# Optimization experiments

Hardware: AMD Instinct MI355X
Metric: run time of the kernel (lower is better)

The kernel has to match this reference:

```python
import jax, jax.numpy as jnp
import numpy as np

N_NODES = 50000
DEG = 32
HEADS = 4
OUT_F = 16
IN_F = 64
NEG_SLOPE = 0.01  # jax.nn.leaky_relu default


def setup_inputs() -> dict:
    key = jax.random.key(0)
    k_adj, k_mask, k_q, k_qw, k_kw, k_aw = jax.random.split(key, 6)
    adj = jax.random.randint(k_adj, (N_NODES, DEG), 0, N_NODES)
    pad = jax.random.uniform(k_mask, (N_NODES, DEG)) < 0.1
    adj = jnp.where(pad, -1, adj)
    Q = jax.random.normal(k_q, (IN_F, N_NODES), dtype=jnp.float32)
    qw_scale = 2 * np.sqrt(6.0 / (IN_F + OUT_F * HEADS))
    kw_scale = qw_scale
    a_scale = 2 * np.sqrt(6.0 / (OUT_F + HEADS))
    query_weight = (jax.random.uniform(k_qw, (HEADS, OUT_F, IN_F)) - 0.5) * qw_scale
    key_weight = (jax.random.uniform(k_kw, (HEADS, OUT_F, IN_F)) - 0.5) * kw_scale
    attn_weight = (jax.random.uniform(k_aw, (HEADS, OUT_F)) - 0.5) * a_scale
    return {
        'adj': adj,
        'Q': Q,
        'query_weight': query_weight.astype(jnp.float32),
        'key_weight': key_weight.astype(jnp.float32),
        'attn_weight': attn_weight.astype(jnp.float32),
    }


def reference(adj, Q, query_weight, key_weight, attn_weight):
    # K defaults to Q (self-attention over graph)
    K = Q
    # project keys: [H, O, N], then gather neighbors -> [H, O, N, deg]
    Ko = jnp.einsum('hoi,in->hon', key_weight, K)[..., adj]
    # project queries: [H, O, N]
    Qo = jnp.einsum('hoi,in->hon', query_weight, Q)
    # per-edge pre-activation and attention logits
    X = jax.nn.leaky_relu(Qo[..., None] + Ko, negative_slope=NEG_SLOPE)
    X = jnp.einsum('honk,ho->hnk', X, attn_weight)  # [H, N, deg]
    X = jnp.where(adj == -1, -jnp.inf, X)
    # rows with zero valid neighbors -> zero logits (uniform softmax, masked later)
    X = jnp.where((adj != -1).sum(-1, keepdims=True) == 0, 0.0, X)
    attn = jax.nn.softmax(X, axis=-1)
    # weighted aggregate of gathered keys -> [H, O, N]
    return jnp.einsum('hnk,honk->hon', jnp.where(adj == -1, 0.0, attn), Ko)
```

## Files before the change

kernel.cpp:

```cpp
#include <hip/hip_runtime.h>
#include <math.h>

#define DEG 32
#define NHO 64
#define NPW 4
#define NPB 16

typedef short  frag8  __attribute__((ext_vector_type(8)));
typedef float  f32x4  __attribute__((ext_vector_type(4)));

template <int CTRL>
__device__ __forceinline__ float dpp_add(float v) {
    int t = __builtin_amdgcn_update_dpp(0, __float_as_int(v), CTRL, 0xF, 0xF, true);
    return v + __int_as_float(t);
}

__device__ __forceinline__ unsigned bf16_rne(float f) {
    unsigned u = __float_as_uint(f);
    return (u + 0x7fffu + ((u >> 16) & 1u)) >> 16;
}

__global__ __launch_bounds__(256) void proj_mfma_kernel(
    const float* __restrict__ Q,
    const float* __restrict__ Wq,
    const float* __restrict__ Wk,
    unsigned short* __restrict__ Pqb,
    unsigned short* __restrict__ Pkb,
    int N)
{
    __shared__ unsigned qlds[64 * 33];
    __shared__ unsigned wlds[128 * 33];

    int t  = threadIdx.x;
    int n0 = blockIdx.x * 64;

    {
        int l    = t >> 1;
        int half = t & 1;
        const float* wr = (l < 64 ? Wq + (size_t)l * 64
                                  : Wk + (size_t)(l - 64) * 64) + half * 32;
#pragma unroll
        for (int r = 0; r < 16; r++) {
            float f0 = wr[2 * r], f1 = wr[2 * r + 1];
            wlds[l * 33 + half * 16 + r] = bf16_rne(f0) | (bf16_rne(f1) << 16);
        }
    }
    {
        int n  = t & 63;
        int gn = n0 + n;
        bool act = (gn < N);
#pragma unroll
        for (int r = 0; r < 8; r++) {
            int dp = (t >> 6) * 8 + r;
            int k  = dp * 2;
            float f0 = act ? Q[(size_t)k * N + gn] : 0.f;
            float f1 = act ? Q[(size_t)(k + 1) * N + gn] : 0.f;
            qlds[n * 33 + dp] = bf16_rne(f0) | (bf16_rne(f1) << 16);
        }
    }
    __syncthreads();

    int lane = t & 63;
    int w    = t >> 6;
    int li   = lane & 15;
    int quad = lane >> 4;

    f32x4 acc[8];
#pragma unroll
    for (int ot = 0; ot < 8; ot++) acc[ot] = (f32x4){0.f, 0.f, 0.f, 0.f};

#pragma unroll
    for (int ks = 0; ks < 2; ks++) {
        union { unsigned u[4]; frag8 f; } A;
        int abase = (w * 16 + li) * 33 + ks * 16 + quad * 4;
#pragma unroll
        for (int c = 0; c < 4; c++) A.u[c] = qlds[abase + c];
#pragma unroll
        for (int ot = 0; ot < 8; ot++) {
            union { unsigned u[4]; frag8 f; } B;
            int bbase = (ot * 16 + li) * 33 + ks * 16 + quad * 4;
#pragma unroll
            for (int c = 0; c < 4; c++) B.u[c] = wlds[bbase + c];
            acc[ot] = __builtin_amdgcn_mfma_f32_16x16x32_bf16(A.f, B.f, acc[ot],
                                                              0, 0, 0);
        }
    }

#pragma unroll
    for (int ot = 0; ot < 8; ot++) {
#pragma unroll
        for (int r = 0; r < 4; r++) {
            int node = n0 + w * 16 + quad * 4 + r;
            if (node < N) {
                unsigned short v = (unsigned short)bf16_rne(acc[ot][r]);
                if (ot < 4)
                    Pqb[(size_t)node * NHO + ot * 16 + li] = v;
                else
                    Pkb[(size_t)node * NHO + (ot - 4) * 16 + li] = v;
            }
        }
    }
}

__global__ __launch_bounds__(256) void gat_kernel(
    const int*            __restrict__ adj,
    const unsigned short* __restrict__ Pqb,
    const unsigned short* __restrict__ Pkb,
    const float*          __restrict__ aw,
    float*                __restrict__ out,
    int N)
{
    __shared__ float tile[NHO][NPB + 1];

    int l    = threadIdx.x & 63;
    int wv   = threadIdx.x >> 6;
    int sl   = l & 15;
    int slot = l >> 4;

    const uint2* Pk64 = (const uint2*)Pkb;
    const uint2* Pq64 = (const uint2*)Pqb;

    float4 awq = *(const float4*)(aw + 4 * sl);
    const float L2E = 1.44269504f;
    float c1_0 = 0.505f * L2E * awq.x, c2_0 = 0.495f * L2E * awq.x;
    float c1_1 = 0.505f * L2E * awq.y, c2_1 = 0.495f * L2E * awq.y;
    float c1_2 = 0.505f * L2E * awq.z, c2_2 = 0.495f * L2E * awq.z;
    float c1_3 = 0.505f * L2E * awq.w, c2_3 = 0.495f * L2E * awq.w;

    int bprm_x16 = (l ^ 16) * 4;
    int bprm_x32 = (l ^ 32) * 4;

    int nbase = blockIdx.x * NPB + wv * NPW;

#pragma unroll 1
    for (int ni = 0; ni < NPW; ni++) {
        int n = nbase + ni;
        if (n < N) {
            uint2 qraw = Pq64[(size_t)n * 16 + sl];
            float qp0 = __uint_as_float(qraw.x << 16);
            float qp1 = __uint_as_float(qraw.x & 0xffff0000u);
            float qp2 = __uint_as_float(qraw.y << 16);
            float qp3 = __uint_as_float(qraw.y & 0xffff0000u);
            int adjA  = adj[(size_t)n * DEG + (l & 31)];

            float c1q = c1_0 * qp0;
            c1q = fmaf(c1_1, qp1, c1q);
            c1q = fmaf(c1_2, qp2, c1q);
            c1q = fmaf(c1_3, qp3, c1q);

            int   jv[8];
            uint2 kvr[8];
#pragma unroll
            for (int t = 0; t < 8; t++) {
                int j = __builtin_amdgcn_ds_bpermute((slot * 8 + t) * 4, adjA);
                jv[t] = j;
                kvr[t] = Pk64[(size_t)(j < 0 ? 0 : j) * 16 + sl];
            }

            float s = 0.f, a0 = 0.f, a1 = 0.f, a2 = 0.f, a3 = 0.f;
#pragma unroll
            for (int t = 0; t < 8; t++) {
                float kv0 = __uint_as_float(kvr[t].x << 16);
                float kv1 = __uint_as_float(kvr[t].x & 0xffff0000u);
                float kv2 = __uint_as_float(kvr[t].y << 16);
                float kv3 = __uint_as_float(kvr[t].y & 0xffff0000u);
                float x0 = qp0 + kv0, x1 = qp1 + kv1;
                float x2 = qp2 + kv2, x3 = qp3 + kv3;
                float c = fmaf(c1_0, kv0, c1q);
                c = fmaf(c1_1, kv1, c);
                c = fmaf(c1_2, kv2, c);
                c = fmaf(c1_3, kv3, c);
                c = fmaf(c2_0, fabsf(x0), c);
                c = fmaf(c2_1, fabsf(x1), c);
                c = fmaf(c2_2, fabsf(x2), c);
                c = fmaf(c2_3, fabsf(x3), c);
                c = dpp_add<0xB1>(c);
                c = dpp_add<0x4E>(c);
                float p = __builtin_amdgcn_exp2f(c);
                p = (jv[t] >= 0) ? p : 0.f;
                s += p;
                a0 = fmaf(p, kv0, a0);
                a1 = fmaf(p, kv1, a1);
                a2 = fmaf(p, kv2, a2);
                a3 = fmaf(p, kv3, a3);
            }

            s  += __int_as_float(__builtin_amdgcn_ds_bpermute(bprm_x16, __float_as_int(s)));
            a0 += __int_as_float(__builtin_amdgcn_ds_bpermute(bprm_x16, __float_as_int(a0)));
            a1 += __int_as_float(__builtin_amdgcn_ds_bpermute(bprm_x16, __float_as_int(a1)));
            a2 += __int_as_float(__builtin_amdgcn_ds_bpermute(bprm_x16, __float_as_int(a2)));
            a3 += __int_as_float(__builtin_amdgcn_ds_bpermute(bprm_x16, __float_as_int(a3)));
            s  += __int_as_float(__builtin_amdgcn_ds_bpermute(bprm_x32, __float_as_int(s)));
            a0 += __int_as_float(__builtin_amdgcn_ds_bpermute(bprm_x32, __float_as_int(a0)));
            a1 += __int_as_float(__builtin_amdgcn_ds_bpermute(bprm_x32, __float_as_int(a1)));
            a2 += __int_as_float(__builtin_amdgcn_ds_bpermute(bprm_x32, __float_as_int(a2)));
            a3 += __int_as_float(__builtin_amdgcn_ds_bpermute(bprm_x32, __float_as_int(a3)));

            float rs = (s > 0.f) ? __builtin_amdgcn_rcpf(s) : 0.f;
            if (slot == 0) {
                int col = wv * NPW + ni;
                tile[4 * sl + 0][col] = a0 * rs;
                tile[4 * sl + 1][col] = a1 * rs;
                tile[4 * sl + 2][col] = a2 * rs;
                tile[4 * sl + 3][col] = a3 * rs;
            }
        }
    }
    __syncthreads();

    int n0 = blockIdx.x * NPB;
    int lr = threadIdx.x >> 2;
    int c4 = threadIdx.x & 3;
    int nc = n0 + c4 * 4;
    float4 v = make_float4(tile[lr][c4 * 4 + 0], tile[lr][c4 * 4 + 1],
                           tile[lr][c4 * 4 + 2], tile[lr][c4 * 4 + 3]);
    if (nc + 3 < N) {
        *(float4*)(out + (size_t)lr * N + nc) = v;
    } else {
#pragma unroll
        for (int e = 0; e < 4; e++)
            if (nc + e < N) out[(size_t)lr * N + nc + e] = (&v.x)[e];
    }
}

extern "C" void kernel_launch(void* const* d_in, const int* in_sizes, int n_in,
                              void* d_out, int out_size, void* d_ws, size_t ws_size,
                              hipStream_t stream) {
    const int*   adj = (const int*)  d_in[0];
    const float* Q   = (const float*)d_in[1];
    const float* qw  = (const float*)d_in[2];
    const float* kw  = (const float*)d_in[3];
    const float* aw  = (const float*)d_in[4];
    float*       out = (float*)d_out;

    int N = in_sizes[0] / DEG;

    unsigned short* Pqb = (unsigned short*)d_ws;
    unsigned short* Pkb = Pqb + (size_t)N * NHO;

    proj_mfma_kernel<<<(N + 63) / 64, 256, 0, stream>>>(Q, qw, kw, Pqb, Pkb, N);

    gat_kernel<<<(N + NPB - 1) / NPB, 256, 0, stream>>>(adj, Pqb, Pkb, aw, out, N);
}
```

Measured before the change: 109.5 us.

## Double-buffer neighbor gathers and load adjacency as int4 in GAT kernel

The per-wave node loop is unrolled and the neighbor key gathers are double-buffered, so the next node's Pk loads are in flight while the current node computes. Adjacency indices are now loaded directly as two int4 vectors per lane instead of one scalar load followed by eight ds_bpermute shuffles. The xor-16 reduction step uses ds_swizzle instead of bpermute, and launch bounds request 4 blocks per CU. The cost is higher register pressure from the two 8-entry gather buffers and the preloaded indices, which could limit occupancy.

```diff
diff --git a/kernel.cpp b/kernel.cpp
--- a/kernel.cpp
+++ b/kernel.cpp
@@ -102,7 +102,96 @@
     }
 }
 
-__global__ __launch_bounds__(256) void gat_kernel(
+
+__device__ __forceinline__ float swz_x16(float v) {
+    return __int_as_float(__builtin_amdgcn_ds_swizzle(__float_as_int(v), 0x401F));
+}
+__device__ __forceinline__ float bprm(int addr, float v) {
+    return __int_as_float(__builtin_amdgcn_ds_bpermute(addr, __float_as_int(v)));
+}
+
+__device__ __forceinline__ void gat_gather(uint2 (&dst)[8],
+                                           const int4 lo, const int4 hi,
+                                           const uint2* __restrict__ Pk64,
+                                           int sl) {
+    dst[0] = Pk64[(size_t)(lo.x < 0 ? 0 : lo.x) * 16 + sl];
+    dst[1] = Pk64[(size_t)(lo.y < 0 ? 0 : lo.y) * 16 + sl];
+    dst[2] = Pk64[(size_t)(lo.z < 0 ? 0 : lo.z) * 16 + sl];
+    dst[3] = Pk64[(size_t)(lo.w < 0 ? 0 : lo.w) * 16 + sl];
+    dst[4] = Pk64[(size_t)(hi.x < 0 ? 0 : hi.x) * 16 + sl];
+    dst[5] = Pk64[(size_t)(hi.y < 0 ? 0 : hi.y) * 16 + sl];
+    dst[6] = Pk64[(size_t)(hi.z < 0 ? 0 : hi.z) * 16 + sl];
+    dst[7] = Pk64[(size_t)(hi.w < 0 ? 0 : hi.w) * 16 + sl];
+}
+
+__device__ __forceinline__ void gat_compute(
+    const uint2 (&kv)[8], const int4 lo, const int4 hi, uint2 qraw,
+    float c1_0, float c1_1, float c1_2, float c1_3,
+    float c2_0, float c2_1, float c2_2, float c2_3,
+    int slot, int sl, int bprm_x32, int col,
+    float (&tile)[NHO][NPB + 1])
+{
+    float qp0 = __uint_as_float(qraw.x << 16);
+    float qp1 = __uint_as_float(qraw.x & 0xffff0000u);
+    float qp2 = __uint_as_float(qraw.y << 16);
+    float qp3 = __uint_as_float(qraw.y & 0xffff0000u);
+
+    float c1q = c1_0 * qp0;
+    c1q = fmaf(c1_1, qp1, c1q);
+    c1q = fmaf(c1_2, qp2, c1q);
+    c1q = fmaf(c1_3, qp3, c1q);
+
+    const int jt[8] = {lo.x, lo.y, lo.z, lo.w, hi.x, hi.y, hi.z, hi.w};
+
+    float s = 0.f, a0 = 0.f, a1 = 0.f, a2 = 0.f, a3 = 0.f;
+#pragma unroll
+    for (int t = 0; t < 8; t++) {
+        float kv0 = __uint_as_float(kv[t].x << 16);
+        float kv1 = __uint_as_float(kv[t].x & 0xffff0000u);
+        float kv2 = __uint_as_float(kv[t].y << 16);
+        float kv3 = __uint_as_float(kv[t].y & 0xffff0000u);
+        float x0 = qp0 + kv0, x1 = qp1 + kv1;
+        float x2 = qp2 + kv2, x3 = qp3 + kv3;
+        float c = fmaf(c1_0, kv0, c1q);
+        c = fmaf(c1_1, kv1, c);
+        c = fmaf(c1_2, kv2, c);
+        c = fmaf(c1_3, kv3, c);
+        c = fmaf(c2_0, fabsf(x0), c);
+        c = fmaf(c2_1, fabsf(x1), c);
+        c = fmaf(c2_2, fabsf(x2), c);
+        c = fmaf(c2_3, fabsf(x3), c);
+        c = dpp_add<0xB1>(c);
+        c = dpp_add<0x4E>(c);
+        float p = __builtin_amdgcn_exp2f(c);
+        p = (jt[t] >= 0) ? p : 0.f;
+        s += p;
+        a0 = fmaf(p, kv0, a0);
+        a1 = fmaf(p, kv1, a1);
+        a2 = fmaf(p, kv2, a2);
+        a3 = fmaf(p, kv3, a3);
+    }
+
+    s  += swz_x16(s);
+    a0 += swz_x16(a0);
+    a1 += swz_x16(a1);
+    a2 += swz_x16(a2);
+    a3 += swz_x16(a3);
+    s  += bprm(bprm_x32, s);
+    a0 += bprm(bprm_x32, a0);
+    a1 += bprm(bprm_x32, a1);
+    a2 += bprm(bprm_x32, a2);
+    a3 += bprm(bprm_x32, a3);
+
+    float rs = (s > 0.f) ? __builtin_amdgcn_rcpf(s) : 0.f;
+    if (slot == 0) {
+        tile[4 * sl + 0][col] = a0 * rs;
+        tile[4 * sl + 1][col] = a1 * rs;
+        tile[4 * sl + 2][col] = a2 * rs;
+        tile[4 * sl + 3][col] = a3 * rs;
+    }
+}
+
+__global__ __launch_bounds__(256, 4) void gat_kernel(
     const int*            __restrict__ adj,
     const unsigned short* __restrict__ Pqb,
     const unsigned short* __restrict__ Pkb,
@@ -127,82 +216,54 @@
     float c1_2 = 0.505f * L2E * awq.z, c2_2 = 0.495f * L2E * awq.z;
     float c1_3 = 0.505f * L2E * awq.w, c2_3 = 0.495f * L2E * awq.w;
 
-    int bprm_x16 = (l ^ 16) * 4;
     int bprm_x32 = (l ^ 32) * 4;
-
     int nbase = blockIdx.x * NPB + wv * NPW;
 
+    if (nbase + NPW <= N) {
+        int4  aLo[NPW], aHi[NPW];
+        uint2 qr[NPW];
+#pragma unroll
+        for (int ni = 0; ni < NPW; ni++) {
+            const int* ap = adj + (size_t)(nbase + ni) * DEG + slot * 8;
+            aLo[ni] = *(const int4*)ap;
+            aHi[ni] = *(const int4*)(ap + 4);
+            qr[ni]  = Pq64[(size_t)(nbase + ni) * 16 + sl];
+        }
+
+        uint2 kvA[8], kvB[8];
+        gat_gather(kvA, aLo[0], aHi[0], Pk64, sl);
+
+#pragma unroll
+        for (int ni = 0; ni < NPW; ni++) {
+            int col = wv * NPW + ni;
+            if ((ni & 1) == 0) {
+                if (ni + 1 < NPW)
+                    gat_gather(kvB, aLo[ni + 1], aHi[ni + 1], Pk64, sl);
+                gat_compute(kvA, aLo[ni], aHi[ni], qr[ni],
+                            c1_0, c1_1, c1_2, c1_3, c2_0, c2_1, c2_2, c2_3,
+                            slot, sl, bprm_x32, col, tile);
+            } else {
+                if (ni + 1 < NPW)
+                    gat_gather(kvA, aLo[ni + 1], aHi[ni + 1], Pk64, sl);
+                gat_compute(kvB, aLo[ni], aHi[ni], qr[ni],
+                            c1_0, c1_1, c1_2, c1_3, c2_0, c2_1, c2_2, c2_3,
+                            slot, sl, bprm_x32, col, tile);
+            }
+        }
+    } else {
+        uint2 kvA[8];
 #pragma unroll 1
-    for (int ni = 0; ni < NPW; ni++) {
-        int n = nbase + ni;
-        if (n < N) {
-            uint2 qraw = Pq64[(size_t)n * 16 + sl];
-            float qp0 = __uint_as_float(qraw.x << 16);
-            float qp1 = __uint_as_float(qraw.x & 0xffff0000u);
-            float qp2 = __uint_as_float(qraw.y << 16);
-            float qp3 = __uint_as_float(qraw.y & 0xffff0000u);
-            int adjA  = adj[(size_t)n * DEG + (l & 31)];
-
-            float c1q = c1_0 * qp0;
-            c1q = fmaf(c1_1, qp1, c1q);
-            c1q = fmaf(c1_2, qp2, c1q);
-            c1q = fmaf(c1_3, qp3, c1q);
-
-            int   jv[8];
-            uint2 kvr[8];
-#pragma unroll
-            for (int t = 0; t < 8; t++) {
-                int j = __builtin_amdgcn_ds_bpermute((slot * 8 + t) * 4, adjA);
-                jv[t] = j;
-                kvr[t] = Pk64[(size_t)(j < 0 ? 0 : j) * 16 + sl];
-            }
-
-            float s = 0.f, a0 = 0.f, a1 = 0.f, a2 = 0.f, a3 = 0.f;
-#pragma unroll
-            for (int t = 0; t < 8; t++) {
-                float kv0 = __uint_as_float(kvr[t].x << 16);
-                float kv1 = __uint_as_float(kvr[t].x & 0xffff0000u);
-                float kv2 = __uint_as_float(kvr[t].y << 16);
-                float kv3 = __uint_as_float(kvr[t].y & 0xffff0000u);
-                float x0 = qp0 + kv0, x1 = qp1 + kv1;
-                float x2 = qp2 + kv2, x3 = qp3 + kv3;
-                float c = fmaf(c1_0, kv0, c1q);
-                c = fmaf(c1_1, kv1, c);
-                c = fmaf(c1_2, kv2, c);
-                c = fmaf(c1_3, kv3, c);
-                c = fmaf(c2_0, fabsf(x0), c);
-                c = fmaf(c2_1, fabsf(x1), c);
-                c = fmaf(c2_2, fabsf(x2), c);
-                c = fmaf(c2_3, fabsf(x3), c);
-                c = dpp_add<0xB1>(c);
-                c = dpp_add<0x4E>(c);
-                float p = __builtin_amdgcn_exp2f(c);
-                p = (jv[t] >= 0) ? p : 0.f;
-                s += p;
-                a0 = fmaf(p, kv0, a0);
-                a1 = fmaf(p, kv1, a1);
-                a2 = fmaf(p, kv2, a2);
-                a3 = fmaf(p, kv3, a3);
-            }
-
-            s  += __int_as_float(__builtin_amdgcn_ds_bpermute(bprm_x16, __float_as_int(s)));
-            a0 += __int_as_float(__builtin_amdgcn_ds_bpermute(bprm_x16, __float_as_int(a0)));
-            a1 += __int_as_float(__builtin_amdgcn_ds_bpermute(bprm_x16, __float_as_int(a1)));
-            a2 += __int_as_float(__builtin_amdgcn_ds_bpermute(bprm_x16, __float_as_int(a2)));
-            a3 += __int_as_float(__builtin_amdgcn_ds_bpermute(bprm_x16, __float_as_int(a3)));
-            s  += __int_as_float(__builtin_amdgcn_ds_bpermute(bprm_x32, __float_as_int(s)));
-            a0 += __int_as_float(__builtin_amdgcn_ds_bpermute(bprm_x32, __float_as_int(a0)));
-            a1 += __int_as_float(__builtin_amdgcn_ds_bpermute(bprm_x32, __float_as_int(a1)));
-            a2 += __int_as_float(__builtin_amdgcn_ds_bpermute(bprm_x32, __float_as_int(a2)));
-            a3 += __int_as_float(__builtin_amdgcn_ds_bpermute(bprm_x32, __float_as_int(a3)));
-
-            float rs = (s > 0.f) ? __builtin_amdgcn_rcpf(s) : 0.f;
-            if (slot == 0) {
-                int col = wv * NPW + ni;
-                tile[4 * sl + 0][col] = a0 * rs;
-                tile[4 * sl + 1][col] = a1 * rs;
-                tile[4 * sl + 2][col] = a2 * rs;
-                tile[4 * sl + 3][col] = a3 * rs;
+        for (int ni = 0; ni < NPW; ni++) {
+            int n = nbase + ni;
+            if (n < N) {
+                const int* ap = adj + (size_t)n * DEG + slot * 8;
+                int4 lo = *(const int4*)ap;
+                int4 hi = *(const int4*)(ap + 4);
+                uint2 qraw = Pq64[(size_t)n * 16 + sl];
+                gat_gather(kvA, lo, hi, Pk64, sl);
+                gat_compute(kvA, lo, hi, qraw,
+                            c1_0, c1_1, c1_2, c1_3, c2_0, c2_1, c2_2, c2_3,
+                            slot, sl, bprm_x32, wv * NPW + ni, tile);
             }
         }
     }
```

Result: faster. 106.4 us (-2.8%).
